# Kernel tuning notes

Hardware: AMD Instinct MI355X
Metric: run time of the kernel (lower is better)

## Reference

```python
import jax, jax.numpy as jnp
import numpy as np

B, NM, MB, D = 16, 64, 64, 1024
NH, NKV, MEM = 16, 8, 64
HD = D // NH            # 64
S = MB + MEM            # per-step attention length
EPS = 1e-6

def precompute_freqs_cis(dim, end, theta=10000.0):
    freqs = 1.0 / (theta ** (jnp.arange(0, dim, 2)[: dim // 2].astype(jnp.float32) / dim))
    t = jnp.arange(end, dtype=jnp.float32)
    return jnp.exp(1j * jnp.outer(t, freqs))  # [end, dim//2] complex64

def apply_rope(x, fcis):
    # x: [s, h, d], fcis: [s, d//2] complex
    xc = x.reshape(x.shape[0], x.shape[1], HD // 2, 2)
    xc = jax.lax.complex(xc[..., 0], xc[..., 1]) * fcis[:, None, :]
    return jnp.stack([jnp.real(xc), jnp.imag(xc)], axis=-1).reshape(x.shape)

def layer_norm(x, scale, bias):
    m = x.mean(-1, keepdims=True)
    v = x.var(-1, keepdims=True)
    return (x - m) * jax.lax.rsqrt(v + EPS) * scale + bias

def setup_inputs() -> dict:
    key = jax.random.key(0)
    ks = jax.random.split(key, 8)
    s = 1.0 / np.sqrt(D)
    return {
        'hidden_states': jax.random.normal(ks[0], (B, NM, MB, D), jnp.float32),
        'mask': jax.random.bernoulli(ks[1], 0.9, (B, NM)),
        'mem_state': jax.random.normal(ks[2], (MEM, D), jnp.float32) * s,
        'wq': jax.random.normal(ks[3], (D, D), jnp.float32) * s,
        'wk': jax.random.normal(ks[4], (D, NKV * HD), jnp.float32) * s,
        'wv': jax.random.normal(ks[5], (D, NKV * HD), jnp.float32) * s,
        'wo': jax.random.normal(ks[6], (D, D), jnp.float32) * s,
        'pre_scale': jnp.ones((D,), jnp.float32),
        'pre_bias': jnp.zeros((D,), jnp.float32),
        'post_scale': jnp.ones((D,), jnp.float32),
        'post_bias': jnp.zeros((D,), jnp.float32),
    }

def reference(hidden_states, mask, mem_state, wq, wk, wv, wo, pre_scale, pre_bias, post_scale, post_bias):
    fcis = precompute_freqs_cis(HD, S)  # constant RoPE buffer, first S positions used
    rep = NH // NKV
    scale = 1.0 / np.sqrt(HD)

    def step(mem, inp):
        x_mb, m = inp  # x_mb: [MB, D], m: scalar bool
        h = layer_norm(jnp.concatenate([x_mb, mem], axis=0), pre_scale, pre_bias)  # [S, D]
        q = (h @ wq).reshape(S, NH, HD)
        k = (h @ wk).reshape(S, NKV, HD)
        v = (h @ wv).reshape(S, NKV, HD)
        q = apply_rope(q, fcis)
        k = apply_rope(k, fcis)
        k = jnp.repeat(k, rep, axis=1)  # GQA: expand kv heads
        v = jnp.repeat(v, rep, axis=1)
        qb, kb, vb = q.astype(jnp.bfloat16), k.astype(jnp.bfloat16), v.astype(jnp.bfloat16)
        logits = jnp.einsum('qhd,khd->hqk', qb, kb).astype(jnp.float32) * scale
        att = jax.nn.softmax(logits, axis=-1).astype(jnp.bfloat16)
        enc = jnp.einsum('hqk,khd->qhd', att, vb).reshape(S, D).astype(jnp.float32)
        out = enc[-MEM:] @ wo  # only memory-slot queries feed the update
        new_mem = layer_norm(out + mem, post_scale, post_bias)
        new_mem = jnp.where(m, new_mem, mem)  # lax.cond branch as select
        return new_mem, None

    def per_batch(x, m):
        final, _ = jax.lax.scan(step, mem_state, (x, m))
        return final

    return jax.vmap(per_batch)(hidden_states, mask)  # [B, MEM, D]
```

## Files before the change

kernel.cpp:

```cpp
#include <hip/hip_runtime.h>


typedef __attribute__((ext_vector_type(8))) _Float16 f16x8;
typedef __attribute__((ext_vector_type(4))) _Float16 f16x4;
typedef __attribute__((ext_vector_type(8))) short    s16x8;
typedef __attribute__((ext_vector_type(4))) float    f32x4;

#define NB   16
#define NMs  64
#define MBs  64
#define Dm   1024
#define NHh  16
#define NKVh 8
#define HDd  64
#define MEMm 64
#define Sq   128

__device__ __align__(16) _Float16      g_W1t[2048 * 1024];
__device__ __align__(16) _Float16      g_Wot[1024 * 1024];
__device__ __align__(16) float         g_rc[128 * 32];
__device__ __align__(16) float         g_rs[128 * 32];
__device__                unsigned char g_mask[NB * NMs];
__device__ __align__(16) _Float16      g_hx[(size_t)NB * NMs * MBs * Dm];
__device__ __align__(16) _Float16      g_hmem[NB * MEMm * Dm];
__device__ __align__(16) float         g_mem[NB * MEMm * Dm];
__device__ __align__(16) unsigned short g_qb[NB * NHh * 64 * 64];
__device__ __align__(16) unsigned short g_kb[NB * NKVh * 128 * 64];
__device__ __align__(16) unsigned short g_vt[NB * NKVh * 64 * 128];
__device__ __align__(16) _Float16      g_enc[NB * 64 * Dm];
__device__ __align__(16) float         g_outp[NB * 64 * Dm];

__device__ __forceinline__ unsigned short f2bf(float x) {
    union { float f; unsigned u; } v; v.f = x;
    unsigned u = v.u;
    return (unsigned short)((u + 0x7fffu + ((u >> 16) & 1u)) >> 16);
}
__device__ __forceinline__ float bf2f(unsigned short h) {
    union { unsigned u; float f; } v; v.u = ((unsigned)h) << 16; return v.f;
}

__device__ __forceinline__ void block_stats(float s, float ss, float eps,
                                            float* mean, float* rstd) {
    for (int off = 32; off > 0; off >>= 1) {
        s  += __shfl_down(s, off);
        ss += __shfl_down(ss, off);
    }
    __shared__ float red[8];
    int wid = threadIdx.x >> 6, lane = threadIdx.x & 63;
    __syncthreads();
    if (lane == 0) { red[wid] = s; red[4 + wid] = ss; }
    __syncthreads();
    float ts  = red[0] + red[1] + red[2] + red[3];
    float tss = red[4] + red[5] + red[6] + red[7];
    float m   = ts * (1.0f / 1024.0f);
    float var = tss * (1.0f / 1024.0f) - m * m;
    *mean = m;
    *rstd = rsqrtf(var + eps);
}

__global__ void k_transpose(const float* __restrict__ in, int ncols, int dsel) {
    _Float16* out = (dsel == 0) ? g_W1t
                  : (dsel == 1) ? (g_W1t + 1024 * 1024)
                  : (dsel == 2) ? (g_W1t + 1536 * 1024)
                                : g_Wot;
    __shared__ float tile[64][65];
    int bk = blockIdx.x, bn = blockIdx.y;
    int c = threadIdx.x & 63, rg = threadIdx.x >> 6;
    int k0 = bk * 64, n0 = bn * 64;
    for (int i = 0; i < 16; i++) {
        int r = rg * 16 + i;
        tile[r][c] = in[(size_t)(k0 + r) * ncols + n0 + c];
    }
    __syncthreads();
    for (int i = 0; i < 16; i++) {
        int r = rg * 16 + i;
        out[(size_t)(n0 + r) * 1024 + k0 + c] = (_Float16)tile[c][r];
    }
}

__global__ void k_rope() {
    int t = threadIdx.x;
    for (int j = 0; j < 32; j++) {
        double f = pow(10000.0, -(double)j / 32.0);
        double a = (double)t * f;
        g_rc[t * 32 + j] = (float)cos(a);
        g_rs[t * 32 + j] = (float)sin(a);
    }
}

__global__ void k_mask(const unsigned int* __restrict__ ip) {
    __shared__ int byteFmt;
    int t = threadIdx.x;
    if (t == 0) byteFmt = 0;
    __syncthreads();
    if (t < 256) {
        unsigned v = ip[t];
        if (!(v == 0u || v == 1u || v == 0x3F800000u)) byteFmt = 1;
    }
    __syncthreads();
    unsigned char m = byteFmt ? (((const unsigned char*)ip)[t] != 0)
                              : (ip[t] != 0u);
    g_mask[t] = m;
}

__global__ void k_ln_hx(const float* __restrict__ x,
                        const float* __restrict__ sc, const float* __restrict__ bi) {
    size_t row = blockIdx.x;
    int t = threadIdx.x;
    float4 v = ((const float4*)(x + row * 1024))[t];
    float mean, rstd;
    block_stats(v.x + v.y + v.z + v.w,
                v.x * v.x + v.y * v.y + v.z * v.z + v.w * v.w, 1e-6f, &mean, &rstd);
    float4 s4 = ((const float4*)sc)[t];
    float4 b4 = ((const float4*)bi)[t];
    f16x4 o;
    o[0] = (_Float16)((v.x - mean) * rstd * s4.x + b4.x);
    o[1] = (_Float16)((v.y - mean) * rstd * s4.y + b4.y);
    o[2] = (_Float16)((v.z - mean) * rstd * s4.z + b4.z);
    o[3] = (_Float16)((v.w - mean) * rstd * s4.w + b4.w);
    *(f16x4*)(g_hx + row * 1024 + t * 4) = o;
}

__global__ void k_ln_init(const float* __restrict__ ms,
                          const float* __restrict__ sc, const float* __restrict__ bi) {
    int b = blockIdx.x >> 6, r = blockIdx.x & 63;
    int t = threadIdx.x;
    float4 v = ((const float4*)(ms + (size_t)r * 1024))[t];
    ((float4*)(g_mem + ((size_t)b * 64 + r) * 1024))[t] = v;
    float mean, rstd;
    block_stats(v.x + v.y + v.z + v.w,
                v.x * v.x + v.y * v.y + v.z * v.z + v.w * v.w, 1e-6f, &mean, &rstd);
    float4 s4 = ((const float4*)sc)[t];
    float4 b4 = ((const float4*)bi)[t];
    f16x4 o;
    o[0] = (_Float16)((v.x - mean) * rstd * s4.x + b4.x);
    o[1] = (_Float16)((v.y - mean) * rstd * s4.y + b4.y);
    o[2] = (_Float16)((v.z - mean) * rstd * s4.z + b4.z);
    o[3] = (_Float16)((v.w - mean) * rstd * s4.w + b4.w);
    *(f16x4*)(g_hmem + ((size_t)b * 64 + r) * 1024 + t * 4) = o;
}

__device__ __forceinline__ void gemm_core(const _Float16* __restrict__ Abase,
                                          const _Float16* __restrict__ Bbase,
                                          _Float16* As, _Float16* Bs,
                                          f32x4 acc[2][2]) {
    int tid = threadIdx.x;
    int w = tid >> 6, l = tid & 63;
    int mo = (w & 1) * 32, no = (w >> 1) * 32;
    int sr = tid >> 2, sk = (tid & 3) * 8;
    int fr = l & 15, fq = (l >> 4) * 8;
    for (int kt = 0; kt < 32; ++kt) {
        f16x8 av = *(const f16x8*)(Abase + (size_t)sr * 1024 + kt * 32 + sk);
        f16x8 bv = *(const f16x8*)(Bbase + (size_t)sr * 1024 + kt * 32 + sk);
        __syncthreads();
        *(f16x8*)&As[sr * 40 + sk] = av;
        *(f16x8*)&Bs[sr * 40 + sk] = bv;
        __syncthreads();
        f16x8 a0 = *(const f16x8*)&As[(mo + fr) * 40 + fq];
        f16x8 a1 = *(const f16x8*)&As[(mo + 16 + fr) * 40 + fq];
        f16x8 b0 = *(const f16x8*)&Bs[(no + fr) * 40 + fq];
        f16x8 b1 = *(const f16x8*)&Bs[(no + 16 + fr) * 40 + fq];
        acc[0][0] = __builtin_amdgcn_mfma_f32_16x16x32_f16(a0, b0, acc[0][0], 0, 0, 0);
        acc[0][1] = __builtin_amdgcn_mfma_f32_16x16x32_f16(a0, b1, acc[0][1], 0, 0, 0);
        acc[1][0] = __builtin_amdgcn_mfma_f32_16x16x32_f16(a1, b0, acc[1][0], 0, 0, 0);
        acc[1][1] = __builtin_amdgcn_mfma_f32_16x16x32_f16(a1, b1, acc[1][1], 0, 0, 0);
    }
}

__launch_bounds__(256)
__global__ void k_gemm1(int s) {
    int bid = blockIdx.x;
    int b = bid / 48, t48 = bid % 48;
    if (!g_mask[b * 64 + s]) return;
    int mtile = (t48 < 16) ? 0 : 1;
    int ntile = (t48 < 16) ? (16 + t48) : (t48 - 16);
    const _Float16* Abase = (mtile == 0)
        ? (g_hx + ((size_t)(b * NMs + s) * 64) * 1024)
        : (g_hmem + (size_t)b * 64 * 1024);
    const _Float16* Bbase = g_W1t + (size_t)ntile * 64 * 1024;
    __shared__ __align__(16) _Float16 As[64 * 40];
    __shared__ __align__(16) _Float16 Bs[64 * 40];
    f32x4 acc[2][2] = {};
    gemm_core(Abase, Bbase, As, Bs, acc);

    int tid = threadIdx.x, w = tid >> 6, l = tid & 63;
    int mo = (w & 1) * 32, no = (w >> 1) * 32;
    int quad = l >> 4, col = l & 15;
    int m0 = mtile * 64 + mo;
    int n0 = ntile * 64 + no;
    for (int i = 0; i < 2; i++)
        for (int j = 0; j < 2; j++)
            for (int r = 0; r < 4; r++) {
                float val = acc[i][j][r];
                float p = __shfl_xor(val, 1);
                int m = m0 + i * 16 + quad * 4 + r;
                int n = n0 + j * 16 + col;
                int d = n & 63;
                if (ntile < 16) {
                    int jj = d >> 1;
                    float c = g_rc[m * 32 + jj], sn = g_rs[m * 32 + jj];
                    float o = (d & 1) ? (p * sn + val * c) : (val * c - p * sn);
                    g_qb[(((size_t)b * 16 + ntile) * 64 + (m - 64)) * 64 + d] = f2bf(o);
                } else if (ntile < 24) {
                    int kvh = ntile - 16;
                    int jj = d >> 1;
                    float c = g_rc[m * 32 + jj], sn = g_rs[m * 32 + jj];
                    float o = (d & 1) ? (p * sn + val * c) : (val * c - p * sn);
                    g_kb[(((size_t)b * 8 + kvh) * 128 + m) * 64 + d] = f2bf(o);
                } else {
                    int kvh = ntile - 24;
                    g_vt[(((size_t)b * 8 + kvh) * 64 + d) * 128 + m] = f2bf(val);
                }
            }
}

__launch_bounds__(256)
__global__ void k_attn(int s) {
    int b = blockIdx.x >> 4, h = blockIdx.x & 15, kvh = h >> 1;
    if (!g_mask[b * 64 + s]) return;
    int tid = threadIdx.x, w = tid >> 6, l = tid & 63;
    int fr = l & 15, fq = (l >> 4) * 8;
    const unsigned short* qp = g_qb + ((size_t)b * 16 + h) * 64 * 64;
    const unsigned short* kp = g_kb + ((size_t)b * 8 + kvh) * 128 * 64;
    const unsigned short* vp = g_vt + ((size_t)b * 8 + kvh) * 64 * 128;

    s16x8 aq0 = *(const s16x8*)(qp + (w * 16 + fr) * 64 + fq);
    s16x8 aq1 = *(const s16x8*)(qp + (w * 16 + fr) * 64 + 32 + fq);
    f32x4 sc[8];
    for (int nt = 0; nt < 8; nt++) {
        sc[nt] = (f32x4){0.f, 0.f, 0.f, 0.f};
        s16x8 kb0 = *(const s16x8*)(kp + (nt * 16 + fr) * 64 + fq);
        s16x8 kb1 = *(const s16x8*)(kp + (nt * 16 + fr) * 64 + 32 + fq);
        sc[nt] = __builtin_amdgcn_mfma_f32_16x16x32_bf16(aq0, kb0, sc[nt], 0, 0, 0);
        sc[nt] = __builtin_amdgcn_mfma_f32_16x16x32_bf16(aq1, kb1, sc[nt], 0, 0, 0);
    }
    float lv[8][4];
    for (int nt = 0; nt < 8; nt++)
        for (int r = 0; r < 4; r++)
            lv[nt][r] = bf2f(f2bf(sc[nt][r])) * 0.125f;

    int quad = l >> 4;
    __shared__ __align__(16) unsigned short att_s[64 * 136];
    for (int r = 0; r < 4; r++) {
        float mx = -1e30f;
        for (int nt = 0; nt < 8; nt++) mx = fmaxf(mx, lv[nt][r]);
        for (int off = 1; off < 16; off <<= 1) mx = fmaxf(mx, __shfl_xor(mx, off));
        float sm = 0.f;
        for (int nt = 0; nt < 8; nt++) { lv[nt][r] = expf(lv[nt][r] - mx); sm += lv[nt][r]; }
        for (int off = 1; off < 16; off <<= 1) sm += __shfl_xor(sm, off);
        float inv = 1.0f / sm;
        int row = w * 16 + quad * 4 + r;
        for (int nt = 0; nt < 8; nt++)
            att_s[row * 136 + nt * 16 + fr] = f2bf(lv[nt][r] * inv);
    }
    f32x4 o[4];
    for (int nt = 0; nt < 4; nt++) o[nt] = (f32x4){0.f, 0.f, 0.f, 0.f};
    for (int kt = 0; kt < 4; kt++) {
        s16x8 a = *(const s16x8*)&att_s[(w * 16 + fr) * 136 + kt * 32 + fq];
        for (int nt = 0; nt < 4; nt++) {
            s16x8 bv = *(const s16x8*)(vp + (nt * 16 + fr) * 128 + kt * 32 + fq);
            o[nt] = __builtin_amdgcn_mfma_f32_16x16x32_bf16(a, bv, o[nt], 0, 0, 0);
        }
    }
    for (int nt = 0; nt < 4; nt++)
        for (int r = 0; r < 4; r++) {
            int m = w * 16 + quad * 4 + r;
            int d = nt * 16 + fr;
            g_enc[((size_t)b * 64 + m) * 1024 + h * 64 + d] =
                (_Float16)bf2f(f2bf(o[nt][r]));
        }
}

__launch_bounds__(256)
__global__ void k_gemm2(int s) {
    int b = blockIdx.x >> 4, ntile = blockIdx.x & 15;
    if (!g_mask[b * 64 + s]) return;
    const _Float16* Abase = g_enc + (size_t)b * 64 * 1024;
    const _Float16* Bbase = g_Wot + (size_t)ntile * 64 * 1024;
    __shared__ __align__(16) _Float16 As[64 * 40];
    __shared__ __align__(16) _Float16 Bs[64 * 40];
    f32x4 acc[2][2] = {};
    gemm_core(Abase, Bbase, As, Bs, acc);

    int tid = threadIdx.x, w = tid >> 6, l = tid & 63;
    int mo = (w & 1) * 32, no = (w >> 1) * 32;
    int quad = l >> 4, col = l & 15;
    for (int i = 0; i < 2; i++)
        for (int j = 0; j < 2; j++)
            for (int r = 0; r < 4; r++) {
                int m = mo + i * 16 + quad * 4 + r;
                int n = ntile * 64 + no + j * 16 + col;
                g_outp[((size_t)b * 64 + m) * 1024 + n] = acc[i][j][r];
            }
}

__global__ void k_ln2(int s, float* __restrict__ dout,
                      const float* __restrict__ psc, const float* __restrict__ pbi,
                      const float* __restrict__ qsc, const float* __restrict__ qbi) {
    int b = blockIdx.x >> 6, r = blockIdx.x & 63;
    int t = threadIdx.x;
    size_t row = (size_t)b * 64 + r;
    if (!g_mask[b * 64 + s]) {
        if (s == NMs - 1)
            ((float4*)(dout + row * 1024))[t] = ((const float4*)(g_mem + row * 1024))[t];
        return;
    }
    float4 ov = ((const float4*)(g_outp + row * 1024))[t];
    float4 mv = ((const float4*)(g_mem + row * 1024))[t];
    float4 y = {ov.x + mv.x, ov.y + mv.y, ov.z + mv.z, ov.w + mv.w};
    float mean, rstd;
    block_stats(y.x + y.y + y.z + y.w,
                y.x * y.x + y.y * y.y + y.z * y.z + y.w * y.w, 1e-6f, &mean, &rstd);
    float4 s4 = ((const float4*)psc)[t];
    float4 b4 = ((const float4*)pbi)[t];
    float4 nm = {(y.x - mean) * rstd * s4.x + b4.x,
                 (y.y - mean) * rstd * s4.y + b4.y,
                 (y.z - mean) * rstd * s4.z + b4.z,
                 (y.w - mean) * rstd * s4.w + b4.w};
    ((float4*)(g_mem + row * 1024))[t] = nm;
    if (s == NMs - 1)
        ((float4*)(dout + row * 1024))[t] = nm;
    float m2, rs2;
    block_stats(nm.x + nm.y + nm.z + nm.w,
                nm.x * nm.x + nm.y * nm.y + nm.z * nm.z + nm.w * nm.w,
                1e-6f, &m2, &rs2);
    float4 c4 = ((const float4*)qsc)[t];
    float4 d4 = ((const float4*)qbi)[t];
    f16x4 o;
    o[0] = (_Float16)((nm.x - m2) * rs2 * c4.x + d4.x);
    o[1] = (_Float16)((nm.y - m2) * rs2 * c4.y + d4.y);
    o[2] = (_Float16)((nm.z - m2) * rs2 * c4.z + d4.z);
    o[3] = (_Float16)((nm.w - m2) * rs2 * c4.w + d4.w);
    *(f16x4*)(g_hmem + row * 1024 + t * 4) = o;
}

extern "C" void kernel_launch(void* const* d_in, const int* in_sizes, int n_in,
                              void* d_out, int out_size, void* d_ws, size_t ws_size,
                              hipStream_t stream) {
    (void)in_sizes; (void)n_in; (void)d_ws; (void)ws_size; (void)out_size;
    const float* hidden    = (const float*)d_in[0];
    const unsigned int* mk = (const unsigned int*)d_in[1];
    const float* mem_state = (const float*)d_in[2];
    const float* wq  = (const float*)d_in[3];
    const float* wk  = (const float*)d_in[4];
    const float* wv  = (const float*)d_in[5];
    const float* wo  = (const float*)d_in[6];
    const float* pre_s  = (const float*)d_in[7];
    const float* pre_b  = (const float*)d_in[8];
    const float* post_s = (const float*)d_in[9];
    const float* post_b = (const float*)d_in[10];
    float* out = (float*)d_out;

    k_transpose<<<dim3(16, 16), 256, 0, stream>>>(wq, 1024, 0);
    k_transpose<<<dim3(16, 8),  256, 0, stream>>>(wk, 512, 1);
    k_transpose<<<dim3(16, 8),  256, 0, stream>>>(wv, 512, 2);
    k_transpose<<<dim3(16, 16), 256, 0, stream>>>(wo, 1024, 3);
    k_rope<<<1, 128, 0, stream>>>();
    k_mask<<<1, 1024, 0, stream>>>(mk);
    k_ln_hx<<<NB * NMs * MBs, 256, 0, stream>>>(hidden, pre_s, pre_b);
    k_ln_init<<<NB * MEMm, 256, 0, stream>>>(mem_state, pre_s, pre_b);

    for (int s = 0; s < NMs; ++s) {
        k_gemm1<<<NB * 48, 256, 0, stream>>>(s);
        k_attn<<<NB * NHh, 256, 0, stream>>>(s);
        k_gemm2<<<NB * 16, 256, 0, stream>>>(s);
        k_ln2<<<NB * MEMm, 256, 0, stream>>>(s, out, post_s, post_b, pre_s, pre_b);
    }
}
```

Measured before the change: 4.050 ms.

## Precompute K/V for all input microbatches in one big batched GEMM

```diff
diff --git a/kernel.cpp b/kernel.cpp
--- a/kernel.cpp
+++ b/kernel.cpp
@@ -24,9 +24,11 @@
 __device__ __align__(16) _Float16      g_hx[(size_t)NB * NMs * MBs * Dm];
 __device__ __align__(16) _Float16      g_hmem[NB * MEMm * Dm];
 __device__ __align__(16) float         g_mem[NB * MEMm * Dm];
+__device__ __align__(16) unsigned short g_kbs[(size_t)1024 * 8 * 64 * 64];
+__device__ __align__(16) unsigned short g_vts[(size_t)1024 * 8 * 64 * 64];
 __device__ __align__(16) unsigned short g_qb[NB * NHh * 64 * 64];
-__device__ __align__(16) unsigned short g_kb[NB * NKVh * 128 * 64];
-__device__ __align__(16) unsigned short g_vt[NB * NKVh * 64 * 128];
+__device__ __align__(16) unsigned short g_kbm[NB * NKVh * 64 * 64];
+__device__ __align__(16) unsigned short g_vtm[NB * NKVh * 64 * 64];
 __device__ __align__(16) _Float16      g_enc[NB * 64 * Dm];
 __device__ __align__(16) float         g_outp[NB * 64 * Dm];
 
@@ -138,6 +140,75 @@
     o[2] = (_Float16)((v.z - mean) * rstd * s4.z + b4.z);
     o[3] = (_Float16)((v.w - mean) * rstd * s4.w + b4.w);
     *(f16x4*)(g_hmem + ((size_t)b * 64 + r) * 1024 + t * 4) = o;
+}
+
+__launch_bounds__(256)
+__global__ void k_kv_big() {
+    int bid = blockIdx.x;
+    int mt = bid >> 3, ntb = bid & 7;
+    size_t m0 = (size_t)mt * 128;
+    int n0 = ntb * 128;
+    const _Float16* Ab = g_hx;
+    const _Float16* Bb = g_W1t + (size_t)1024 * 1024;
+    __shared__ __align__(16) _Float16 As[128 * 40];
+    __shared__ __align__(16) _Float16 Bs[128 * 40];
+    int tid = threadIdx.x;
+    int w = tid >> 6, l = tid & 63;
+    int wr = w >> 1, wc = w & 1;
+    int fr = l & 15, fq = (l >> 4) * 8;
+    int sr = tid >> 2, sk = (tid & 3) * 8;
+    f32x4 acc[4][4] = {};
+    for (int kt = 0; kt < 32; ++kt) {
+        f16x8 a0 = *(const f16x8*)(Ab + (m0 + sr) * 1024 + kt * 32 + sk);
+        f16x8 a1 = *(const f16x8*)(Ab + (m0 + 64 + sr) * 1024 + kt * 32 + sk);
+        f16x8 b0 = *(const f16x8*)(Bb + (size_t)(n0 + sr) * 1024 + kt * 32 + sk);
+        f16x8 b1 = *(const f16x8*)(Bb + (size_t)(n0 + 64 + sr) * 1024 + kt * 32 + sk);
+        __syncthreads();
+        *(f16x8*)&As[sr * 40 + sk] = a0;
+        *(f16x8*)&As[(64 + sr) * 40 + sk] = a1;
+        *(f16x8*)&Bs[sr * 40 + sk] = b0;
+        *(f16x8*)&Bs[(64 + sr) * 40 + sk] = b1;
+        __syncthreads();
+        f16x8 af[4], bf[4];
+#pragma unroll
+        for (int mf = 0; mf < 4; mf++) af[mf] = *(const f16x8*)&As[(wr * 64 + mf * 16 + fr) * 40 + fq];
+#pragma unroll
+        for (int nf = 0; nf < 4; nf++) bf[nf] = *(const f16x8*)&Bs[(wc * 64 + nf * 16 + fr) * 40 + fq];
+#pragma unroll
+        for (int mf = 0; mf < 4; mf++)
+#pragma unroll
+            for (int nf = 0; nf < 4; nf++)
+                acc[mf][nf] = __builtin_amdgcn_mfma_f32_16x16x32_f16(af[mf], bf[nf], acc[mf][nf], 0, 0, 0);
+    }
+    int quad = l >> 4, col = l & 15;
+    if (ntb < 4) {
+        for (int mf = 0; mf < 4; mf++)
+            for (int nf = 0; nf < 4; nf++)
+                for (int r = 0; r < 4; r++) {
+                    float val = acc[mf][nf][r];
+                    float p = __shfl_xor(val, 1);
+                    size_t mg = m0 + wr * 64 + mf * 16 + quad * 4 + r;
+                    size_t g = mg >> 6;
+                    int xr = (int)(mg & 63);
+                    int ng = n0 + wc * 64 + nf * 16 + col;
+                    int kvh = ng >> 6, d = ng & 63, jj = d >> 1;
+                    float c = g_rc[xr * 32 + jj], sn = g_rs[xr * 32 + jj];
+                    float o = (d & 1) ? (p * sn + val * c) : (val * c - p * sn);
+                    g_kbs[((g * 8 + kvh) * 64 + xr) * 64 + d] = f2bf(o);
+                }
+    } else {
+        for (int mf = 0; mf < 4; mf++)
+            for (int nf = 0; nf < 4; nf++)
+                for (int r = 0; r < 4; r++) {
+                    float val = acc[mf][nf][r];
+                    size_t mg = m0 + wr * 64 + mf * 16 + quad * 4 + r;
+                    size_t g = mg >> 6;
+                    int xr = (int)(mg & 63);
+                    int nv = n0 + wc * 64 + nf * 16 + col - 512;
+                    int kvh = nv >> 6, d = nv & 63;
+                    g_vts[((g * 8 + kvh) * 64 + d) * 64 + xr] = f2bf(val);
+                }
+    }
 }
 
 __device__ __forceinline__ void gemm_core(const _Float16* __restrict__ Abase,
@@ -170,13 +241,9 @@
 __launch_bounds__(256)
 __global__ void k_gemm1(int s) {
     int bid = blockIdx.x;
-    int b = bid / 48, t48 = bid % 48;
+    int b = bid >> 5, ntile = bid & 31;
     if (!g_mask[b * 64 + s]) return;
-    int mtile = (t48 < 16) ? 0 : 1;
-    int ntile = (t48 < 16) ? (16 + t48) : (t48 - 16);
-    const _Float16* Abase = (mtile == 0)
-        ? (g_hx + ((size_t)(b * NMs + s) * 64) * 1024)
-        : (g_hmem + (size_t)b * 64 * 1024);
+    const _Float16* Abase = g_hmem + (size_t)b * 64 * 1024;
     const _Float16* Bbase = g_W1t + (size_t)ntile * 64 * 1024;
     __shared__ __align__(16) _Float16 As[64 * 40];
     __shared__ __align__(16) _Float16 Bs[64 * 40];
@@ -186,7 +253,7 @@
     int tid = threadIdx.x, w = tid >> 6, l = tid & 63;
     int mo = (w & 1) * 32, no = (w >> 1) * 32;
     int quad = l >> 4, col = l & 15;
-    int m0 = mtile * 64 + mo;
+    int m0 = 64 + mo;
     int n0 = ntile * 64 + no;
     for (int i = 0; i < 2; i++)
         for (int j = 0; j < 2; j++)
@@ -206,10 +273,10 @@
                     int jj = d >> 1;
                     float c = g_rc[m * 32 + jj], sn = g_rs[m * 32 + jj];
                     float o = (d & 1) ? (p * sn + val * c) : (val * c - p * sn);
-                    g_kb[(((size_t)b * 8 + kvh) * 128 + m) * 64 + d] = f2bf(o);
+                    g_kbm[(((size_t)b * 8 + kvh) * 64 + (m - 64)) * 64 + d] = f2bf(o);
                 } else {
                     int kvh = ntile - 24;
-                    g_vt[(((size_t)b * 8 + kvh) * 64 + d) * 128 + m] = f2bf(val);
+                    g_vtm[(((size_t)b * 8 + kvh) * 64 + d) * 64 + (m - 64)] = f2bf(val);
                 }
             }
 }
@@ -220,17 +287,21 @@
     if (!g_mask[b * 64 + s]) return;
     int tid = threadIdx.x, w = tid >> 6, l = tid & 63;
     int fr = l & 15, fq = (l >> 4) * 8;
-    const unsigned short* qp = g_qb + ((size_t)b * 16 + h) * 64 * 64;
-    const unsigned short* kp = g_kb + ((size_t)b * 8 + kvh) * 128 * 64;
-    const unsigned short* vp = g_vt + ((size_t)b * 8 + kvh) * 64 * 128;
+    const unsigned short* qp  = g_qb  + ((size_t)b * 16 + h) * 64 * 64;
+    const unsigned short* kps = g_kbs + ((size_t)(b * 64 + s) * 8 + kvh) * 4096;
+    const unsigned short* kpm = g_kbm + ((size_t)b * 8 + kvh) * 4096;
+    const unsigned short* vps = g_vts + ((size_t)(b * 64 + s) * 8 + kvh) * 4096;
+    const unsigned short* vpm = g_vtm + ((size_t)b * 8 + kvh) * 4096;
 
     s16x8 aq0 = *(const s16x8*)(qp + (w * 16 + fr) * 64 + fq);
     s16x8 aq1 = *(const s16x8*)(qp + (w * 16 + fr) * 64 + 32 + fq);
     f32x4 sc[8];
     for (int nt = 0; nt < 8; nt++) {
         sc[nt] = (f32x4){0.f, 0.f, 0.f, 0.f};
-        s16x8 kb0 = *(const s16x8*)(kp + (nt * 16 + fr) * 64 + fq);
-        s16x8 kb1 = *(const s16x8*)(kp + (nt * 16 + fr) * 64 + 32 + fq);
+        const unsigned short* kr = (nt < 4) ? (kps + (nt * 16 + fr) * 64)
+                                            : (kpm + ((nt - 4) * 16 + fr) * 64);
+        s16x8 kb0 = *(const s16x8*)(kr + fq);
+        s16x8 kb1 = *(const s16x8*)(kr + 32 + fq);
         sc[nt] = __builtin_amdgcn_mfma_f32_16x16x32_bf16(aq0, kb0, sc[nt], 0, 0, 0);
         sc[nt] = __builtin_amdgcn_mfma_f32_16x16x32_bf16(aq1, kb1, sc[nt], 0, 0, 0);
     }
@@ -257,8 +328,10 @@
     for (int nt = 0; nt < 4; nt++) o[nt] = (f32x4){0.f, 0.f, 0.f, 0.f};
     for (int kt = 0; kt < 4; kt++) {
         s16x8 a = *(const s16x8*)&att_s[(w * 16 + fr) * 136 + kt * 32 + fq];
+        const unsigned short* vb = (kt < 2) ? (vps + kt * 32 + fq)
+                                            : (vpm + (kt - 2) * 32 + fq);
         for (int nt = 0; nt < 4; nt++) {
-            s16x8 bv = *(const s16x8*)(vp + (nt * 16 + fr) * 128 + kt * 32 + fq);
+            s16x8 bv = *(const s16x8*)(vb + (nt * 16 + fr) * 64);
             o[nt] = __builtin_amdgcn_mfma_f32_16x16x32_bf16(a, bv, o[nt], 0, 0, 0);
         }
     }
@@ -359,9 +432,10 @@
     k_mask<<<1, 1024, 0, stream>>>(mk);
     k_ln_hx<<<NB * NMs * MBs, 256, 0, stream>>>(hidden, pre_s, pre_b);
     k_ln_init<<<NB * MEMm, 256, 0, stream>>>(mem_state, pre_s, pre_b);
+    k_kv_big<<<4096, 256, 0, stream>>>();
 
     for (int s = 0; s < NMs; ++s) {
-        k_gemm1<<<NB * 48, 256, 0, stream>>>(s);
+        k_gemm1<<<NB * 32, 256, 0, stream>>>(s);
         k_attn<<<NB * NHh, 256, 0, stream>>>(s);
         k_gemm2<<<NB * 16, 256, 0, stream>>>(s);
         k_ln2<<<NB * MEMm, 256, 0, stream>>>(s, out, post_s, post_b, pre_s, pre_b);
```

Measured after the change: 3.979 ms. No clear change (-1.8%).
